# Optimization experiments

Measured on AMD Instinct MI355X. Metric: run time of the kernel, lower is better.

The kernel has to match this reference:

```python
import jax, jax.numpy as jnp
import numpy as np

N, D = 4096, 768
TEMPERATURE = 0.05


def setup_inputs() -> dict:
    key = jax.random.key(0)
    k1, k2 = jax.random.split(key)
    scale = 1.0 / jnp.sqrt(jnp.float32(D))  # keep dot/T in exp's safe range
    anchors = jax.random.normal(k1, (N, D), dtype=jnp.float32) * scale
    positives = jax.random.normal(k2, (N, D), dtype=jnp.float32) * scale
    return {"anchors": anchors, "positives": positives}


def reference(anchors, positives):
    # logits[j, i] = dot(anchor_j, positive_i) / T  -- single matmul replaces
    # the O(N^2) python-loop torch.dot calls.
    logits = jnp.einsum("jd,id->ji", anchors, positives) / TEMPERATURE  # [N, N]
    e = jnp.exp(logits)
    # Original code: negative_sum starts at exp(dot(anchor_j, positive_j)/T)
    # (the diagonal) and then adds exp(dot(anchor_j, positive_i)/T) for ALL i
    # (so the own positive is counted twice).
    denom = jnp.diagonal(e) + e.sum(axis=1)  # [N]
    # Original bug: positive_similarity is overwritten inside the inner loop,
    # so the numerator is the similarity to the LAST positive (index N-1).
    log_num = logits[:, -1]  # [N]
    loss = -(log_num - jnp.log(denom))
    return loss.sum()
```

## Files before the change

### kernel.cpp

```cpp
#include <hip/hip_runtime.h>
#include <hip/hip_bf16.h>

#define N 4096
#define D 768
#define LN2 0.69314718055994530942f
#define QSCALE 5.371583f

typedef __attribute__((ext_vector_type(4))) int   i32x4;
typedef __attribute__((ext_vector_type(8))) int   i32x8;
typedef __attribute__((ext_vector_type(4))) float f32x4;

#define EXP2F(x) __builtin_amdgcn_exp2f(x)
#define LOG2F(x) __builtin_amdgcn_logf(x)

#define GLDS16(g, l) __builtin_amdgcn_global_load_lds( \
    (const __attribute__((address_space(1))) void*)(g), \
    (__attribute__((address_space(3))) void*)(l), 16, 0, 0)


__global__ void convert_kernel(const float* __restrict__ A, const float* __restrict__ B,
                               unsigned* __restrict__ Af8, unsigned* __restrict__ Bf8) {
    const int total = N * D / 4;
    int idx = blockIdx.x * blockDim.x + threadIdx.x;
    int stride = gridDim.x * blockDim.x;
    for (int i = idx; i < total; i += stride) {
        float4 a = ((const float4*)A)[i];
        float4 b = ((const float4*)B)[i];
        int pa = __builtin_amdgcn_cvt_pk_fp8_f32(a.x * QSCALE, a.y * QSCALE, 0, 0);
        pa     = __builtin_amdgcn_cvt_pk_fp8_f32(a.z * QSCALE, a.w * QSCALE, pa, 1);
        int pb = __builtin_amdgcn_cvt_pk_fp8_f32(b.x * QSCALE, b.y * QSCALE, 0, 0);
        pb     = __builtin_amdgcn_cvt_pk_fp8_f32(b.z * QSCALE, b.w * QSCALE, pb, 1);
        Af8[i] = (unsigned)pa;
        Bf8[i] = (unsigned)pb;
    }
}

__global__ __launch_bounds__(256) void gemm_kernel(const unsigned char* __restrict__ Af8,
                                                   const unsigned char* __restrict__ Bf8,
                                                   float* __restrict__ partial,
                                                   float* __restrict__ diagS,
                                                   float* __restrict__ lastS) {
    __shared__ __align__(16) unsigned char As[2][128 * 128];
    __shared__ __align__(16) unsigned char Bs[2][128 * 128];
    __shared__ float rowsum2[2][128];

    const int t    = threadIdx.x;
    const int bid  = blockIdx.x;
    const int xcd  = bid & 7;
    const int ii   = bid >> 3;
    const int bRow = ((xcd >> 1) << 3) + (ii >> 4);
    const int bCol = ((xcd & 1) << 4) + (ii & 15);
    const int lane = t & 63;
    const int w    = t >> 6;
    const int wr   = w >> 1;
    const int wc   = w & 1;
    const int lr   = lane & 15;
    const int hi   = lane >> 4;

    const int srow = t >> 3;
    const int sc   = t & 7;
    const int gcv  = sc ^ (srow & 7);
    const size_t aOff = (size_t)(bRow * 128 + srow) * D + gcv * 16;
    const size_t bOff = (size_t)(bCol * 128 + srow) * D + gcv * 16;

    f32x4 acc[4][4] = {};
    const int NT = D / 128;

    union Frag { i32x8 v; i32x4 h[2]; };

#define STAGE(BUF, T) do {                                                              \
    const size_t kb_ = (size_t)(T) * 128;                                               \
    _Pragma("unroll")                                                                   \
    for (int inst = 0; inst < 4; ++inst) {                                              \
        GLDS16(Af8 + aOff + (size_t)inst * 32 * D + kb_, &As[BUF][inst * 4096 + w * 1024]); \
        GLDS16(Bf8 + bOff + (size_t)inst * 32 * D + kb_, &Bs[BUF][inst * 4096 + w * 1024]); \
    }                                                                                   \
} while (0)

#define LDFRAG(DST, ARRBUF, ROW) do {                                                   \
    (DST).h[0] = *(const i32x4*)&(ARRBUF)[(ROW) * 128 + ((hi ^ (lr & 7)) * 16)];        \
    (DST).h[1] = *(const i32x4*)&(ARRBUF)[(ROW) * 128 + (((hi + 4) ^ (lr & 7)) * 16)];  \
} while (0)

#define ITER(CUR, T, VN, DOSTAGE) do {                                                  \
    asm volatile("s_waitcnt vmcnt(" #VN ")" ::: "memory");                              \
    __builtin_amdgcn_s_barrier();                                                       \
    __builtin_amdgcn_sched_barrier(0);                                                  \
    Frag bfr[4];                                                                        \
    _Pragma("unroll")                                                                   \
    for (int nf = 0; nf < 4; ++nf)                                                      \
        LDFRAG(bfr[nf], Bs[CUR], wc * 64 + nf * 16 + lr);                               \
    __builtin_amdgcn_s_setprio(1);                                                      \
    _Pragma("unroll")                                                                   \
    for (int mf = 0; mf < 4; ++mf) {                                                    \
        Frag a8;                                                                        \
        LDFRAG(a8, As[CUR], wr * 64 + mf * 16 + lr);                                    \
        _Pragma("unroll")                                                               \
        for (int nf = 0; nf < 4; ++nf)                                                  \
            acc[mf][nf] = __builtin_amdgcn_mfma_scale_f32_16x16x128_f8f6f4(             \
                a8.v, bfr[nf].v, acc[mf][nf], 0, 0, 0, 0x7F7F7F7F, 0, 0x7F7F7F7F);      \
    }                                                                                   \
    __builtin_amdgcn_s_setprio(0);                                                      \
    asm volatile("s_waitcnt lgkmcnt(0)" ::: "memory");                                  \
    __builtin_amdgcn_sched_barrier(0);                                                  \
    __builtin_amdgcn_s_barrier();                                                       \
    __builtin_amdgcn_sched_barrier(0);                                                  \
    if (DOSTAGE) STAGE(CUR, (T) + 2);                                                   \
} while (0)

    STAGE(0, 0);
    STAGE(1, 1);

    for (int tt = 0; tt < NT - 2; tt += 2) {
        ITER(0, tt,     8, 1);
        ITER(1, tt + 1, 8, 1);
    }
    ITER(0, NT - 2, 8, 0);
    ITER(1, NT - 1, 0, 0);
#undef ITER
#undef LDFRAG
#undef STAGE

    const int rifb = hi * 4;

    if (bRow == bCol && wr == wc) {
        #pragma unroll
        for (int mf = 0; mf < 4; ++mf)
            #pragma unroll
            for (int reg = 0; reg < 4; ++reg)
                if (lr == rifb + reg)
                    diagS[bRow * 128 + wr * 64 + mf * 16 + rifb + reg] = acc[mf][mf][reg];
    }

    if (bCol == (N / 128 - 1) && wc == 1 && lr == 15) {
        #pragma unroll
        for (int mf = 0; mf < 4; ++mf)
            #pragma unroll
            for (int reg = 0; reg < 4; ++reg)
                lastS[bRow * 128 + wr * 64 + mf * 16 + rifb + reg] = acc[mf][3][reg];
    }

    #pragma unroll
    for (int mf = 0; mf < 4; ++mf) {
        #pragma unroll
        for (int reg = 0; reg < 4; ++reg) {
            float s = EXP2F(acc[mf][0][reg]) + EXP2F(acc[mf][1][reg]) +
                      EXP2F(acc[mf][2][reg]) + EXP2F(acc[mf][3][reg]);
            s += __shfl_xor(s, 1);
            s += __shfl_xor(s, 2);
            s += __shfl_xor(s, 4);
            s += __shfl_xor(s, 8);
            if (lr == 0) rowsum2[wc][wr * 64 + mf * 16 + rifb + reg] = s;
        }
    }
    __syncthreads();
    if (t < 128) partial[(size_t)bCol * N + bRow * 128 + t] = rowsum2[0][t] + rowsum2[1][t];
}

__global__ void rowloss_kernel(const float* __restrict__ partial, const float* __restrict__ diagS,
                               const float* __restrict__ lastS, float* __restrict__ blockSums) {
    const int j = blockIdx.x * 128 + threadIdx.x;
    float rs = 0.0f;
    #pragma unroll
    for (int tI = 0; tI < 32; ++tI) rs += partial[(size_t)tI * N + j];
    float denom = rs + EXP2F(diagS[j]);
    float lossj = LN2 * (LOG2F(denom) - lastS[j]);
    #pragma unroll
    for (int off = 1; off < 64; off <<= 1) lossj += __shfl_xor(lossj, off);
    __shared__ float ws2[2];
    if ((threadIdx.x & 63) == 0) ws2[threadIdx.x >> 6] = lossj;
    __syncthreads();
    if (threadIdx.x == 0) blockSums[blockIdx.x] = ws2[0] + ws2[1];
}

__global__ void final_kernel(const float* __restrict__ blockSums, float* __restrict__ out) {
    float v = (threadIdx.x < 32) ? blockSums[threadIdx.x] : 0.0f;
    #pragma unroll
    for (int off = 1; off < 32; off <<= 1) v += __shfl_xor(v, off);
    if (threadIdx.x == 0) out[0] = v;
}

extern "C" void kernel_launch(void* const* d_in, const int* in_sizes, int n_in,
                              void* d_out, int out_size, void* d_ws, size_t ws_size,
                              hipStream_t stream) {
    const float* A = (const float*)d_in[0];
    const float* B = (const float*)d_in[1];
    float* out = (float*)d_out;
    char* ws = (char*)d_ws;

    unsigned char* Af8 = (unsigned char*)(ws);
    unsigned char* Bf8 = (unsigned char*)(ws + 3145728);
    float* partial     = (float*)(ws + 6291456);
    float* diagS       = (float*)(ws + 6815744);
    float* lastS       = (float*)(ws + 6832128);
    float* blockSums   = (float*)(ws + 6848512);

    convert_kernel<<<1024, 256, 0, stream>>>(A, B, (unsigned*)Af8, (unsigned*)Bf8);
    gemm_kernel<<<1024, 256, 0, stream>>>(Af8, Bf8, partial, diagS, lastS);
    rowloss_kernel<<<32, 128, 0, stream>>>(partial, diagS, lastS, blockSums);
    final_kernel<<<1, 64, 0, stream>>>(blockSums, out);
}
```

Before: 36.07 us.

## Load B fragments directly from global memory and fuse final reduction via atomics

Each wave now reads its B fragments straight from global memory into registers, and only A is staged through double-buffered LDS. This halves LDS footprint and staging traffic and may raise occupancy. The cost is uncoalesced 16-byte global loads that depend on cache hits and sit on the critical path, since the wait counts cover only A. Separately, the final reduction kernel is removed: the convert kernel zeroes the output and each rowloss block adds its partial with atomicAdd, saving one launch but making the float summation order nondeterministic.

```diff
diff --git a/kernel.cpp b/kernel.cpp
--- a/kernel.cpp
+++ b/kernel.cpp
@@ -19,7 +19,9 @@
 
 
 __global__ void convert_kernel(const float* __restrict__ A, const float* __restrict__ B,
-                               unsigned* __restrict__ Af8, unsigned* __restrict__ Bf8) {
+                               unsigned* __restrict__ Af8, unsigned* __restrict__ Bf8,
+                               float* __restrict__ out) {
+    if (blockIdx.x == 0 && threadIdx.x == 0) out[0] = 0.0f;
     const int total = N * D / 4;
     int idx = blockIdx.x * blockDim.x + threadIdx.x;
     int stride = gridDim.x * blockDim.x;
@@ -41,7 +43,6 @@
                                                    float* __restrict__ diagS,
                                                    float* __restrict__ lastS) {
     __shared__ __align__(16) unsigned char As[2][128 * 128];
-    __shared__ __align__(16) unsigned char Bs[2][128 * 128];
     __shared__ float rowsum2[2][128];
 
     const int t    = threadIdx.x;
@@ -61,25 +62,32 @@
     const int sc   = t & 7;
     const int gcv  = sc ^ (srow & 7);
     const size_t aOff = (size_t)(bRow * 128 + srow) * D + gcv * 16;
-    const size_t bOff = (size_t)(bCol * 128 + srow) * D + gcv * 16;
+
+    const unsigned char* Bbase = Bf8 + (size_t)(bCol * 128 + wc * 64 + lr) * D + hi * 16;
 
     f32x4 acc[4][4] = {};
-    const int NT = D / 128;
 
     union Frag { i32x8 v; i32x4 h[2]; };
 
-#define STAGE(BUF, T) do {                                                              \
+#define STAGE_A(BUF, T) do {                                                            \
     const size_t kb_ = (size_t)(T) * 128;                                               \
     _Pragma("unroll")                                                                   \
-    for (int inst = 0; inst < 4; ++inst) {                                              \
+    for (int inst = 0; inst < 4; ++inst)                                                \
         GLDS16(Af8 + aOff + (size_t)inst * 32 * D + kb_, &As[BUF][inst * 4096 + w * 1024]); \
-        GLDS16(Bf8 + bOff + (size_t)inst * 32 * D + kb_, &Bs[BUF][inst * 4096 + w * 1024]); \
+} while (0)
+
+#define LDFRAG_A(DST, BUF, ROW) do {                                                    \
+    (DST).h[0] = *(const i32x4*)&As[BUF][(ROW) * 128 + ((hi ^ (lr & 7)) * 16)];         \
+    (DST).h[1] = *(const i32x4*)&As[BUF][(ROW) * 128 + (((hi + 4) ^ (lr & 7)) * 16)];   \
+} while (0)
+
+#define LOADB(T) do {                                                                   \
+    const unsigned char* bp_ = Bbase + (size_t)(T) * 128;                               \
+    _Pragma("unroll")                                                                   \
+    for (int nf = 0; nf < 4; ++nf) {                                                    \
+        bfr[nf].h[0] = *(const i32x4*)(bp_ + (size_t)nf * 16 * D);                      \
+        bfr[nf].h[1] = *(const i32x4*)(bp_ + (size_t)nf * 16 * D + 64);                 \
     }                                                                                   \
-} while (0)
-
-#define LDFRAG(DST, ARRBUF, ROW) do {                                                   \
-    (DST).h[0] = *(const i32x4*)&(ARRBUF)[(ROW) * 128 + ((hi ^ (lr & 7)) * 16)];        \
-    (DST).h[1] = *(const i32x4*)&(ARRBUF)[(ROW) * 128 + (((hi + 4) ^ (lr & 7)) * 16)];  \
 } while (0)
 
 #define ITER(CUR, T, VN, DOSTAGE) do {                                                  \
@@ -87,14 +95,12 @@
     __builtin_amdgcn_s_barrier();                                                       \
     __builtin_amdgcn_sched_barrier(0);                                                  \
     Frag bfr[4];                                                                        \
-    _Pragma("unroll")                                                                   \
-    for (int nf = 0; nf < 4; ++nf)                                                      \
-        LDFRAG(bfr[nf], Bs[CUR], wc * 64 + nf * 16 + lr);                               \
+    LOADB(T);                                                                           \
     __builtin_amdgcn_s_setprio(1);                                                      \
     _Pragma("unroll")                                                                   \
     for (int mf = 0; mf < 4; ++mf) {                                                    \
         Frag a8;                                                                        \
-        LDFRAG(a8, As[CUR], wr * 64 + mf * 16 + lr);                                    \
+        LDFRAG_A(a8, CUR, wr * 64 + mf * 16 + lr);                                      \
         _Pragma("unroll")                                                               \
         for (int nf = 0; nf < 4; ++nf)                                                  \
             acc[mf][nf] = __builtin_amdgcn_mfma_scale_f32_16x16x128_f8f6f4(             \
@@ -105,21 +111,22 @@
     __builtin_amdgcn_sched_barrier(0);                                                  \
     __builtin_amdgcn_s_barrier();                                                       \
     __builtin_amdgcn_sched_barrier(0);                                                  \
-    if (DOSTAGE) STAGE(CUR, (T) + 2);                                                   \
-} while (0)
-
-    STAGE(0, 0);
-    STAGE(1, 1);
-
-    for (int tt = 0; tt < NT - 2; tt += 2) {
-        ITER(0, tt,     8, 1);
-        ITER(1, tt + 1, 8, 1);
-    }
-    ITER(0, NT - 2, 8, 0);
-    ITER(1, NT - 1, 0, 0);
+    if (DOSTAGE) STAGE_A(CUR, (T) + 2);                                                 \
+} while (0)
+
+    STAGE_A(0, 0);
+    STAGE_A(1, 1);
+
+    ITER(0, 0, 4, 1);
+    ITER(1, 1, 4, 1);
+    ITER(0, 2, 4, 1);
+    ITER(1, 3, 4, 1);
+    ITER(0, 4, 4, 0);
+    ITER(1, 5, 0, 0);
 #undef ITER
-#undef LDFRAG
-#undef STAGE
+#undef LOADB
+#undef LDFRAG_A
+#undef STAGE_A
 
     const int rifb = hi * 4;
 
@@ -158,7 +165,7 @@
 }
 
 __global__ void rowloss_kernel(const float* __restrict__ partial, const float* __restrict__ diagS,
-                               const float* __restrict__ lastS, float* __restrict__ blockSums) {
+                               const float* __restrict__ lastS, float* __restrict__ out) {
     const int j = blockIdx.x * 128 + threadIdx.x;
     float rs = 0.0f;
     #pragma unroll
@@ -170,14 +177,7 @@
     __shared__ float ws2[2];
     if ((threadIdx.x & 63) == 0) ws2[threadIdx.x >> 6] = lossj;
     __syncthreads();
-    if (threadIdx.x == 0) blockSums[blockIdx.x] = ws2[0] + ws2[1];
-}
-
-__global__ void final_kernel(const float* __restrict__ blockSums, float* __restrict__ out) {
-    float v = (threadIdx.x < 32) ? blockSums[threadIdx.x] : 0.0f;
-    #pragma unroll
-    for (int off = 1; off < 32; off <<= 1) v += __shfl_xor(v, off);
-    if (threadIdx.x == 0) out[0] = v;
+    if (threadIdx.x == 0) atomicAdd(out, ws2[0] + ws2[1]);
 }
 
 extern "C" void kernel_launch(void* const* d_in, const int* in_sizes, int n_in,
@@ -193,10 +193,8 @@
     float* partial     = (float*)(ws + 6291456);
     float* diagS       = (float*)(ws + 6815744);
     float* lastS       = (float*)(ws + 6832128);
-    float* blockSums   = (float*)(ws + 6848512);
-
-    convert_kernel<<<1024, 256, 0, stream>>>(A, B, (unsigned*)Af8, (unsigned*)Bf8);
+
+    convert_kernel<<<1024, 256, 0, stream>>>(A, B, (unsigned*)Af8, (unsigned*)Bf8, out);
     gemm_kernel<<<1024, 256, 0, stream>>>(Af8, Bf8, partial, diagS, lastS);
-    rowloss_kernel<<<32, 128, 0, stream>>>(partial, diagS, lastS, blockSums);
-    final_kernel<<<1, 64, 0, stream>>>(blockSums, out);
-}
+    rowloss_kernel<<<32, 128, 0, stream>>>(partial, diagS, lastS, out);
+}
```

Measured after the change: 48.57 us. 34.7% more time.

## Drop LDS double buffering in GEMM and fold final reduction into atomics

Applied to the files above, without the earlier changes.

The GEMM main loop goes from a two-stage double-buffered LDS pipeline to a single buffer, where each tile waits for its global loads to finish before computing. This halves LDS use, which could raise occupancy, but it removes the overlap between loading and computing. The separate final reduction kernel is also removed: rowloss now atomically adds block sums into the output, which convert_kernel zeroes. That saves one launch but makes the float summation order nondeterministic.

```diff
diff --git a/kernel.cpp b/kernel.cpp
--- a/kernel.cpp
+++ b/kernel.cpp
@@ -19,7 +19,9 @@
 
 
 __global__ void convert_kernel(const float* __restrict__ A, const float* __restrict__ B,
-                               unsigned* __restrict__ Af8, unsigned* __restrict__ Bf8) {
+                               unsigned* __restrict__ Af8, unsigned* __restrict__ Bf8,
+                               float* __restrict__ out) {
+    if (blockIdx.x == 0 && threadIdx.x == 0) out[0] = 0.0f;
     const int total = N * D / 4;
     int idx = blockIdx.x * blockDim.x + threadIdx.x;
     int stride = gridDim.x * blockDim.x;
@@ -40,8 +42,8 @@
                                                    float* __restrict__ partial,
                                                    float* __restrict__ diagS,
                                                    float* __restrict__ lastS) {
-    __shared__ __align__(16) unsigned char As[2][128 * 128];
-    __shared__ __align__(16) unsigned char Bs[2][128 * 128];
+    __shared__ __align__(16) unsigned char As[128 * 128];
+    __shared__ __align__(16) unsigned char Bs[128 * 128];
     __shared__ float rowsum2[2][128];
 
     const int t    = threadIdx.x;
@@ -68,58 +70,43 @@
 
     union Frag { i32x8 v; i32x4 h[2]; };
 
-#define STAGE(BUF, T) do {                                                              \
-    const size_t kb_ = (size_t)(T) * 128;                                               \
-    _Pragma("unroll")                                                                   \
-    for (int inst = 0; inst < 4; ++inst) {                                              \
-        GLDS16(Af8 + aOff + (size_t)inst * 32 * D + kb_, &As[BUF][inst * 4096 + w * 1024]); \
-        GLDS16(Bf8 + bOff + (size_t)inst * 32 * D + kb_, &Bs[BUF][inst * 4096 + w * 1024]); \
-    }                                                                                   \
-} while (0)
-
 #define LDFRAG(DST, ARRBUF, ROW) do {                                                   \
     (DST).h[0] = *(const i32x4*)&(ARRBUF)[(ROW) * 128 + ((hi ^ (lr & 7)) * 16)];        \
     (DST).h[1] = *(const i32x4*)&(ARRBUF)[(ROW) * 128 + (((hi + 4) ^ (lr & 7)) * 16)];  \
 } while (0)
 
-#define ITER(CUR, T, VN, DOSTAGE) do {                                                  \
-    asm volatile("s_waitcnt vmcnt(" #VN ")" ::: "memory");                              \
-    __builtin_amdgcn_s_barrier();                                                       \
-    __builtin_amdgcn_sched_barrier(0);                                                  \
-    Frag bfr[4];                                                                        \
-    _Pragma("unroll")                                                                   \
-    for (int nf = 0; nf < 4; ++nf)                                                      \
-        LDFRAG(bfr[nf], Bs[CUR], wc * 64 + nf * 16 + lr);                               \
-    __builtin_amdgcn_s_setprio(1);                                                      \
-    _Pragma("unroll")                                                                   \
-    for (int mf = 0; mf < 4; ++mf) {                                                    \
-        Frag a8;                                                                        \
-        LDFRAG(a8, As[CUR], wr * 64 + mf * 16 + lr);                                    \
-        _Pragma("unroll")                                                               \
-        for (int nf = 0; nf < 4; ++nf)                                                  \
-            acc[mf][nf] = __builtin_amdgcn_mfma_scale_f32_16x16x128_f8f6f4(             \
-                a8.v, bfr[nf].v, acc[mf][nf], 0, 0, 0, 0x7F7F7F7F, 0, 0x7F7F7F7F);      \
-    }                                                                                   \
-    __builtin_amdgcn_s_setprio(0);                                                      \
-    asm volatile("s_waitcnt lgkmcnt(0)" ::: "memory");                                  \
-    __builtin_amdgcn_sched_barrier(0);                                                  \
-    __builtin_amdgcn_s_barrier();                                                       \
-    __builtin_amdgcn_sched_barrier(0);                                                  \
-    if (DOSTAGE) STAGE(CUR, (T) + 2);                                                   \
-} while (0)
+    for (int tt = 0; tt < NT; ++tt) {
+        const size_t kb = (size_t)tt * 128;
+        #pragma unroll
+        for (int inst = 0; inst < 4; ++inst) {
+            GLDS16(Af8 + aOff + (size_t)inst * 32 * D + kb, &As[inst * 4096 + w * 1024]);
+            GLDS16(Bf8 + bOff + (size_t)inst * 32 * D + kb, &Bs[inst * 4096 + w * 1024]);
+        }
+        asm volatile("s_waitcnt vmcnt(0)" ::: "memory");
+        __builtin_amdgcn_s_barrier();
+        __builtin_amdgcn_sched_barrier(0);
 
-    STAGE(0, 0);
-    STAGE(1, 1);
-
-    for (int tt = 0; tt < NT - 2; tt += 2) {
-        ITER(0, tt,     8, 1);
-        ITER(1, tt + 1, 8, 1);
+        Frag bfr[4];
+        #pragma unroll
+        for (int nf = 0; nf < 4; ++nf)
+            LDFRAG(bfr[nf], Bs, wc * 64 + nf * 16 + lr);
+        __builtin_amdgcn_s_setprio(1);
+        #pragma unroll
+        for (int mf = 0; mf < 4; ++mf) {
+            Frag a8;
+            LDFRAG(a8, As, wr * 64 + mf * 16 + lr);
+            #pragma unroll
+            for (int nf = 0; nf < 4; ++nf)
+                acc[mf][nf] = __builtin_amdgcn_mfma_scale_f32_16x16x128_f8f6f4(
+                    a8.v, bfr[nf].v, acc[mf][nf], 0, 0, 0, 0x7F7F7F7F, 0, 0x7F7F7F7F);
+        }
+        __builtin_amdgcn_s_setprio(0);
+        asm volatile("s_waitcnt lgkmcnt(0)" ::: "memory");
+        __builtin_amdgcn_sched_barrier(0);
+        __builtin_amdgcn_s_barrier();
+        __builtin_amdgcn_sched_barrier(0);
     }
-    ITER(0, NT - 2, 8, 0);
-    ITER(1, NT - 1, 0, 0);
-#undef ITER
 #undef LDFRAG
-#undef STAGE
 
     const int rifb = hi * 4;
 
@@ -158,7 +145,7 @@
 }
 
 __global__ void rowloss_kernel(const float* __restrict__ partial, const float* __restrict__ diagS,
-                               const float* __restrict__ lastS, float* __restrict__ blockSums) {
+                               const float* __restrict__ lastS, float* __restrict__ out) {
     const int j = blockIdx.x * 128 + threadIdx.x;
     float rs = 0.0f;
     #pragma unroll
@@ -170,14 +157,7 @@
     __shared__ float ws2[2];
     if ((threadIdx.x & 63) == 0) ws2[threadIdx.x >> 6] = lossj;
     __syncthreads();
-    if (threadIdx.x == 0) blockSums[blockIdx.x] = ws2[0] + ws2[1];
-}
-
-__global__ void final_kernel(const float* __restrict__ blockSums, float* __restrict__ out) {
-    float v = (threadIdx.x < 32) ? blockSums[threadIdx.x] : 0.0f;
-    #pragma unroll
-    for (int off = 1; off < 32; off <<= 1) v += __shfl_xor(v, off);
-    if (threadIdx.x == 0) out[0] = v;
+    if (threadIdx.x == 0) atomicAdd(out, ws2[0] + ws2[1]);
 }
 
 extern "C" void kernel_launch(void* const* d_in, const int* in_sizes, int n_in,
@@ -193,10 +173,8 @@
     float* partial     = (float*)(ws + 6291456);
     float* diagS       = (float*)(ws + 6815744);
     float* lastS       = (float*)(ws + 6832128);
-    float* blockSums   = (float*)(ws + 6848512);
 
-    convert_kernel<<<1024, 256, 0, stream>>>(A, B, (unsigned*)Af8, (unsigned*)Bf8);
+    convert_kernel<<<1024, 256, 0, stream>>>(A, B, (unsigned*)Af8, (unsigned*)Bf8, out);
     gemm_kernel<<<1024, 256, 0, stream>>>(Af8, Bf8, partial, diagS, lastS);
-    rowloss_kernel<<<32, 128, 0, stream>>>(partial, diagS, lastS, blockSums);
-    final_kernel<<<1, 64, 0, stream>>>(blockSums, out);
+    rowloss_kernel<<<32, 128, 0, stream>>>(partial, diagS, lastS, out);
 }
```

Measured after the change: 34.21 us, median of 2. 5.2% less time.
